# Performance work log

Measured on AMD Instinct MI355X. Metric: run time of the kernel, lower is better.

## Reference

```python
import jax, jax.numpy as jnp
import numpy as np

N_NODES = 100000
N_GRAPHS = 64


def gcn_conv(x, edge_index, edge_weight, W, b):
    # PyG GCNConv: h = W^T x, then out[dst] += norm * h[src], norm = d^-1/2[src]*w*d^-1/2[dst]
    n = x.shape[0]
    loop = jnp.arange(n)
    src = jnp.concatenate([edge_index[0], loop])
    dst = jnp.concatenate([edge_index[1], loop])
    w = jnp.concatenate([edge_weight, jnp.ones((n,), x.dtype)])  # self-loop weight 1
    deg = jax.ops.segment_sum(w, dst, num_segments=n)
    dis = jnp.where(deg > 0, jax.lax.rsqrt(jnp.maximum(deg, 1e-30)), 0.0)
    norm = dis[src] * w * dis[dst]                      # [E+N]
    h = x @ W                                            # [N, d_out]
    msg = h[src] * norm[:, None]                         # gather + scale
    out = jax.ops.segment_sum(msg, dst, num_segments=n)  # scatter-add
    return out + b


def setup_inputs() -> dict:
    key = jax.random.key(0)
    k = jax.random.split(key, 8)
    d_in, d_out = 256, 128
    E = 1600000
    x = jax.random.normal(k[0], (N_NODES, d_in), jnp.float32)
    edge_index = jax.random.randint(k[1], (2, E), 0, N_NODES, jnp.int64)
    edge_weight = jax.random.uniform(k[2], (E,), jnp.float32)
    batch = jnp.sort(jax.random.randint(k[3], (N_NODES,), 0, N_GRAPHS, jnp.int64))
    W_conv = jax.random.normal(k[4], (d_in, d_out), jnp.float32) / np.sqrt(d_in)
    b_conv = jnp.zeros((d_out,), jnp.float32)
    W_lin = jax.random.normal(k[5], (d_out, 1), jnp.float32) / np.sqrt(d_out)
    b_lin = jnp.zeros((1,), jnp.float32)
    return {"x": x, "edge_index": edge_index, "edge_weight": edge_weight,
            "batch": batch, "W_conv": W_conv, "b_conv": b_conv,
            "W_lin": W_lin, "b_lin": b_lin}


def reference(x, edge_index, edge_weight, batch, W_conv, b_conv, W_lin, b_lin):
    h = gcn_conv(x, edge_index, edge_weight, W_conv, b_conv)
    h = jax.nn.relu(h)
    # dropout(p=0.1) treated as identity (eval) for deterministic baseline
    sums = jax.ops.segment_sum(h, batch, num_segments=N_GRAPHS)
    counts = jax.ops.segment_sum(jnp.ones((h.shape[0],), h.dtype), batch,
                                 num_segments=N_GRAPHS)
    pooled = sums / jnp.maximum(counts, 1.0)[:, None]    # [G, d_out]
    logits = pooled @ W_lin + b_lin                       # [G, 1]
    return jax.nn.sigmoid(logits)
```

## Files before the change

kernel.cpp:

```cpp
#include <hip/hip_runtime.h>
#include <hip/hip_bf16.h>
#include <math.h>

#define D_IN 256
#define D_OUT 128
#define WSCALE 1073741824.0f

typedef __bf16 bf16x8 __attribute__((ext_vector_type(8)));
typedef float  f32x4  __attribute__((ext_vector_type(4)));
typedef float  f32x2  __attribute__((ext_vector_type(2)));

__device__ __forceinline__ ushort f2b(float f) {
    unsigned int x = __float_as_uint(f);
    unsigned int r = (x + 0x7FFFu + ((x >> 16) & 1u)) >> 16;
    return (ushort)r;
}
__device__ __forceinline__ f32x2 fp8x2_f32(unsigned u) {
    return __builtin_amdgcn_cvt_pk_f32_fp8(u, false);
}
__device__ __forceinline__ unsigned char f32_fp8(float f) {
    return (unsigned char)(__builtin_amdgcn_cvt_pk_fp8_f32(f, f, 0, false) & 0xFF);
}

__global__ void wt_k(const float* __restrict__ W, ushort* __restrict__ Wtg) {
    int t = blockIdx.x * 256 + threadIdx.x;
    if (t < D_IN * D_OUT) {
        int k = t >> 7, n = t & 127;
        Wtg[n * D_IN + k] = f2b(W[t]);
    }
}

__global__ __launch_bounds__(256, 4) void fused_k(const int* __restrict__ dst,
                                                  const float* __restrict__ w,
                                                  unsigned long long* __restrict__ packed,
                                                  int* __restrict__ pos, int E, int GB,
                                                  const float* __restrict__ X,
                                                  const ushort* __restrict__ Wtg,
                                                  unsigned char* __restrict__ H, int M) {
    const int b = (int)blockIdx.x;
    const bool isg = ((b & 1) == 0) && ((b >> 1) < GB);
    if (!isg) {
        int gb_before = (b + 1) >> 1;
        if (gb_before > GB) gb_before = GB;
        int e0 = (b - gb_before) * 1024 + (int)threadIdx.x;
        #pragma unroll
        for (int i = 0; i < 4; ++i) {
            int e = e0 + i * 256;
            if (e < E) {
                int d = dst[e];
                unsigned long long inc = (1ull << 40) |
                    (unsigned long long)(w[e] * WSCALE);
                unsigned long long old = atomicAdd(&packed[d], inc);
                pos[e] = (int)(old >> 40);
            }
        }
        return;
    }
    extern __shared__ char smem[];
    const int t = threadIdx.x;
    const int brow = (b >> 1) * 64;
    const int wid = t >> 6;
    const int lane = t & 63;
    const int lrow = lane & 15;
    const int lkc = lane >> 4;

    bf16x8 breg[2][8];
    #pragma unroll
    for (int n = 0; n < 2; ++n) {
        int col = wid * 32 + n * 16 + lrow;
        const char* base = (const char*)(Wtg + col * D_IN);
        #pragma unroll
        for (int kk = 0; kk < 8; ++kk)
            breg[n][kk] = *(const bf16x8*)(base + kk * 64 + lkc * 16);
    }

    {
        const float4* x4 = (const float4*)X;
        #pragma unroll
        for (int i = 0; i < 16; ++i) {
            int f = t + 256 * i;
            int row = f >> 6;
            int c4 = f & 63;
            int gr = brow + row;
            if (gr > M - 1) gr = M - 1;
            float4 v = x4[(size_t)gr * 64 + c4];
            ushort4 u;
            u.x = f2b(v.x); u.y = f2b(v.y); u.z = f2b(v.z); u.w = f2b(v.w);
            int phys = row * 512 + (((c4 >> 1) ^ (row & 7)) << 4) + ((c4 & 1) << 3);
            *(ushort4*)(smem + phys) = u;
        }
    }
    __syncthreads();

    f32x4 acc[4][2];
    #pragma unroll
    for (int m = 0; m < 4; ++m)
        #pragma unroll
        for (int n = 0; n < 2; ++n) acc[m][n] = (f32x4){0.f, 0.f, 0.f, 0.f};

    #pragma unroll
    for (int kk = 0; kk < 8; ++kk) {
        bf16x8 a[4];
        #pragma unroll
        for (int m = 0; m < 4; ++m) {
            int row = m * 16 + lrow;
            int chunk = kk * 4 + lkc;
            a[m] = *(const bf16x8*)(smem + row * 512 + ((chunk ^ (row & 7)) << 4));
        }
        #pragma unroll
        for (int m = 0; m < 4; ++m) {
            acc[m][0] = __builtin_amdgcn_mfma_f32_16x16x32_bf16(a[m], breg[0][kk], acc[m][0], 0, 0, 0);
            acc[m][1] = __builtin_amdgcn_mfma_f32_16x16x32_bf16(a[m], breg[1][kk], acc[m][1], 0, 0, 0);
        }
    }

    #pragma unroll
    for (int m = 0; m < 4; ++m) {
        #pragma unroll
        for (int v = 0; v < 4; ++v) {
            int gr = brow + m * 16 + lkc * 4 + v;
            if (gr < M) {
                size_t rb = (size_t)gr * D_OUT;
                H[rb + wid * 32 + lrow]      = f32_fp8(acc[m][0][v]);
                H[rb + wid * 32 + 16 + lrow] = f32_fp8(acc[m][1][v]);
            }
        }
    }
}

__global__ __launch_bounds__(256) void scan1_k(const unsigned long long* __restrict__ packed,
                                               int* __restrict__ row_start,
                                               int* __restrict__ blksum,
                                               float* __restrict__ dis, int N) {
    __shared__ int sdata[256];
    int t = threadIdx.x;
    int base = blockIdx.x * 1024;
    int v[4], s = 0;
    #pragma unroll
    for (int i = 0; i < 4; ++i) {
        int idx = base + t * 4 + i;
        if (idx < N) {
            unsigned long long p = packed[idx];
            int cnt = (int)(p >> 40);
            float deg = 1.0f + (float)(p & ((1ull << 40) - 1)) * (1.0f / WSCALE);
            dis[idx] = rsqrtf(deg);
            v[i] = (cnt + 7) & ~7;
        } else v[i] = 0;
        s += v[i];
    }
    sdata[t] = s;
    __syncthreads();
    #pragma unroll
    for (int off = 1; off < 256; off <<= 1) {
        int x = 0;
        if (t >= off) x = sdata[t - off];
        __syncthreads();
        sdata[t] += x;
        __syncthreads();
    }
    int excl = sdata[t] - s;
    if (t == 255) blksum[blockIdx.x] = sdata[t];
    int run = excl;
    #pragma unroll
    for (int i = 0; i < 4; ++i) {
        int idx = base + t * 4 + i;
        if (idx < N) row_start[idx] = run;
        run += v[i];
    }
}

__global__ __launch_bounds__(256) void scan2_k(const int* __restrict__ blksum,
                                               int* __restrict__ blkpre, int NB,
                                               int* __restrict__ row_start, int N) {
    __shared__ int s[256];
    int t = threadIdx.x;
    int v = (t < NB) ? blksum[t] : 0;
    s[t] = v;
    __syncthreads();
    #pragma unroll
    for (int off = 1; off < 256; off <<= 1) {
        int x = 0;
        if (t >= off) x = s[t - off];
        __syncthreads();
        s[t] += x;
        __syncthreads();
    }
    if (t < NB) blkpre[t] = s[t] - v;
    if (t == NB - 1) row_start[N] = s[t];
}

__global__ void fill_k(const int* __restrict__ src, const int* __restrict__ dst,
                       const float* __restrict__ w, const int* __restrict__ pos,
                       const int* __restrict__ row_start, const int* __restrict__ blkpre,
                       const float* __restrict__ dis,
                       unsigned* __restrict__ csr, int E) {
    int e = blockIdx.x * blockDim.x + threadIdx.x;
    if (e >= E) return;
    int s = src[e];
    int d = dst[e];
    float nm = dis[s] * w[e] * dis[d];
    unsigned rec = ((unsigned)s << 15) | (f2b(nm) & 0x7FFFu);
    csr[row_start[d] + blkpre[d >> 10] + pos[e]] = rec;
}

__global__ __launch_bounds__(256) void agg_pool_k(const int* __restrict__ row_start,
                                                  const int* __restrict__ blkpre,
                                                  const unsigned* __restrict__ csr,
                                                  const unsigned char* __restrict__ h,
                                                  const float* __restrict__ dis,
                                                  const float* __restrict__ bconv,
                                                  const int* __restrict__ batch,
                                                  float* __restrict__ pooled,
                                                  float* __restrict__ counts, int N) {
    int wave = threadIdx.x >> 6;
    int lane = threadIdx.x & 63;
    int c = lane * 2;
    float2 b2 = *(const float2*)&bconv[c];
    int n0 = (blockIdx.x * 4 + wave) * 16;
    if (n0 >= N) return;

    float2 accp = make_float2(0.f, 0.f);
    int curg = -1;
    float gcount = 0.f;

    int nend = n0 + 16;
    if (nend > N) nend = N;

    int rs = row_start[n0] + blkpre[n0 >> 10];

    #pragma unroll 1
    for (int n = n0; n < nend; ++n) {
        int np = n + 1;
        int re = row_start[np] + ((np < N) ? blkpre[np >> 10] : 0);
        float din = dis[n];
        float dn2 = din * din;
        ushort su = *(const ushort*)(h + (size_t)n * D_OUT + c);
        f32x2 sv = fp8x2_f32(su);
        float ax = dn2 * sv[0];
        float ay = dn2 * sv[1];
        #pragma unroll 1
        for (int j = rs; j < re; j += 8) {
            uint4 ra = *(const uint4*)(csr + j);
            uint4 rb = *(const uint4*)(csr + j + 4);
            unsigned rc[8] = {ra.x, ra.y, ra.z, ra.w, rb.x, rb.y, rb.z, rb.w};
            ushort uu[8];
            float nm[8];
            #pragma unroll
            for (int k = 0; k < 8; ++k) {
                nm[k] = __uint_as_float((rc[k] & 0x7FFFu) << 16);
                uu[k] = *(const ushort*)(h + (size_t)((rc[k] >> 15) << 7) + c);
            }
            #pragma unroll
            for (int k = 0; k < 8; ++k) {
                f32x2 hv = fp8x2_f32(uu[k]);
                ax += nm[k] * hv[0];
                ay += nm[k] * hv[1];
            }
        }
        rs = re;
        float vx = fmaxf(ax + b2.x, 0.f);
        float vy = fmaxf(ay + b2.y, 0.f);
        int g = batch[n];
        if (g != curg) {
            if (curg >= 0) {
                atomicAdd(&pooled[curg * D_OUT + c],     accp.x);
                atomicAdd(&pooled[curg * D_OUT + c + 1], accp.y);
                if (lane == 0) atomicAdd(&counts[curg], gcount);
            }
            accp = make_float2(0.f, 0.f);
            gcount = 0.f;
            curg = g;
        }
        accp.x += vx;
        accp.y += vy;
        gcount += 1.f;
    }
    if (curg >= 0) {
        atomicAdd(&pooled[curg * D_OUT + c],     accp.x);
        atomicAdd(&pooled[curg * D_OUT + c + 1], accp.y);
        if (lane == 0) atomicAdd(&counts[curg], gcount);
    }
}

__global__ void head_k(const float* __restrict__ pooled, const float* __restrict__ counts,
                       const float* __restrict__ wlin, const float* __restrict__ blin,
                       float* __restrict__ out, int G) {
    int g = blockIdx.x;
    int lane = threadIdx.x;
    float s = 0.f;
    for (int c = lane; c < D_OUT; c += 64)
        s += pooled[g * D_OUT + c] * wlin[c];
    #pragma unroll
    for (int off = 32; off; off >>= 1) s += __shfl_down(s, off);
    if (lane == 0) {
        float cnt = fmaxf(counts[g], 1.0f);
        float z = s / cnt + blin[0];
        out[g] = 1.0f / (1.0f + expf(-z));
    }
}

extern "C" void kernel_launch(void* const* d_in, const int* in_sizes, int n_in,
                              void* d_out, int out_size, void* d_ws, size_t ws_size,
                              hipStream_t stream) {
    const float* x     = (const float*)d_in[0];
    const int*   ei    = (const int*)  d_in[1];
    const float* ew    = (const float*)d_in[2];
    const int*   batch = (const int*)  d_in[3];
    const float* Wc    = (const float*)d_in[4];
    const float* bc    = (const float*)d_in[5];
    const float* Wl    = (const float*)d_in[6];
    const float* bl    = (const float*)d_in[7];
    float* out = (float*)d_out;

    const int E = in_sizes[2];
    const int N = in_sizes[3];
    const int G = out_size;
    const int NB = (N + 1023) >> 10;
    const int EB = (E + 1023) / 1024;
    const int GB = (N + 63) / 64;
    const int CSR_CAP = E + 8 * N;

    const int* src = ei;
    const int* dst = ei + E;

    unsigned long long* packed = (unsigned long long*)d_ws;
    float*  pooled   = (float*)(packed + N);
    float*  counts   = pooled + (size_t)G * D_OUT;
    unsigned* csr    = (unsigned*)(counts + G);
    int*    pos      = (int*)(csr + CSR_CAP);
    float*  dis      = (float*)(pos + E);
    unsigned char* h = (unsigned char*)(dis + N);
    ushort* Wtg      = (ushort*)(h + (size_t)N * D_OUT);
    int*    row_start= (int*)(Wtg + D_IN * D_OUT);
    int*    blksum   = row_start + N + 1;
    int*    blkpre   = blksum + NB;

    size_t zbytes = (size_t)N * 8 + ((size_t)G * D_OUT + G) * sizeof(float)
                  + (size_t)CSR_CAP * sizeof(unsigned);
    hipMemsetAsync(packed, 0, zbytes, stream);

    wt_k      <<<(D_IN * D_OUT + 255) / 256, 256, 0, stream>>>(Wc, Wtg);

    fused_k   <<<EB + GB, 256, 32768, stream>>>(dst, ew, packed, pos, E, GB,
                                                x, Wtg, h, N);

    scan1_k   <<<NB, 256, 0, stream>>>(packed, row_start, blksum, dis, N);
    scan2_k   <<<1, 256, 0, stream>>>(blksum, blkpre, NB, row_start, N);

    fill_k    <<<(E + 255) / 256, 256, 0, stream>>>(src, dst, ew, pos, row_start, blkpre, dis, csr, E);

    agg_pool_k<<<(N + 63) / 64, 256, 0, stream>>>(row_start, blkpre, csr, h, dis, bc, batch,
                                                  pooled, counts, N);

    head_k    <<<G, 64, 0, stream>>>(pooled, counts, Wl, bl, out, G);
}
```

Before: 210.8 us.

## Replicate degree/count atomics per XCD to keep atomics local to each L2

The degree and count atomic accumulator is replicated once per XCD (eight copies). Each edge block reads its hardware XCC id and does workgroup-scope atomics into its own replica, which avoids cross-die coherence traffic. The scan then merges the eight replicas into per-XCD prefix offsets stored as 16-bit values, and fill_k adds the right offset when placing each CSR entry. This costs an eight-times larger memset and extra reads in the scan. Workgroup scope on global atomics across CUs of the same XCD relies on the shared L2 for correctness, and the 16-bit prefixes assume node degrees stay below 65536.

```diff
diff --git a/kernel.cpp b/kernel.cpp
--- a/kernel.cpp
+++ b/kernel.cpp
@@ -5,6 +5,8 @@
 #define D_IN 256
 #define D_OUT 128
 #define WSCALE 1073741824.0f
+#define NXCD 8
+#define XCC_GETREG_IMM ((31 << 11) | 20)
 
 typedef __bf16 bf16x8 __attribute__((ext_vector_type(8)));
 typedef float  f32x4  __attribute__((ext_vector_type(4)));
@@ -32,7 +34,7 @@
 
 __global__ __launch_bounds__(256, 4) void fused_k(const int* __restrict__ dst,
                                                   const float* __restrict__ w,
-                                                  unsigned long long* __restrict__ packed,
+                                                  unsigned long long* __restrict__ packed8,
                                                   int* __restrict__ pos, int E, int GB,
                                                   const float* __restrict__ X,
                                                   const ushort* __restrict__ Wtg,
@@ -43,6 +45,8 @@
         int gb_before = (b + 1) >> 1;
         if (gb_before > GB) gb_before = GB;
         int e0 = (b - gb_before) * 1024 + (int)threadIdx.x;
+        int xcd = (int)(__builtin_amdgcn_s_getreg(XCC_GETREG_IMM) & 7u);
+        unsigned long long* rep = packed8 + (size_t)xcd * M;
         #pragma unroll
         for (int i = 0; i < 4; ++i) {
             int e = e0 + i * 256;
@@ -50,8 +54,9 @@
                 int d = dst[e];
                 unsigned long long inc = (1ull << 40) |
                     (unsigned long long)(w[e] * WSCALE);
-                unsigned long long old = atomicAdd(&packed[d], inc);
-                pos[e] = (int)(old >> 40);
+                unsigned long long old = __hip_atomic_fetch_add(
+                    &rep[d], inc, __ATOMIC_RELAXED, __HIP_MEMORY_SCOPE_WORKGROUP);
+                pos[e] = (xcd << 27) | (int)(old >> 40);
             }
         }
         return;
@@ -128,10 +133,11 @@
     }
 }
 
-__global__ __launch_bounds__(256) void scan1_k(const unsigned long long* __restrict__ packed,
+__global__ __launch_bounds__(256) void scan1_k(const unsigned long long* __restrict__ packed8,
                                                int* __restrict__ row_start,
                                                int* __restrict__ blksum,
-                                               float* __restrict__ dis, int N) {
+                                               float* __restrict__ dis,
+                                               uint4* __restrict__ xbase, int N) {
     __shared__ int sdata[256];
     int t = threadIdx.x;
     int base = blockIdx.x * 1024;
@@ -140,11 +146,25 @@
     for (int i = 0; i < 4; ++i) {
         int idx = base + t * 4 + i;
         if (idx < N) {
-            unsigned long long p = packed[idx];
-            int cnt = (int)(p >> 40);
-            float deg = 1.0f + (float)(p & ((1ull << 40) - 1)) * (1.0f / WSCALE);
+            unsigned long long ws = 0;
+            unsigned pre[8];
+            unsigned run = 0;
+            #pragma unroll
+            for (int k = 0; k < 8; ++k) {
+                unsigned long long p = packed8[(size_t)k * N + idx];
+                pre[k] = run;
+                run += (unsigned)(p >> 40);
+                ws += p & ((1ull << 40) - 1);
+            }
+            float deg = 1.0f + (float)ws * (1.0f / WSCALE);
             dis[idx] = rsqrtf(deg);
-            v[i] = (cnt + 7) & ~7;
+            uint4 xb;
+            xb.x = pre[0] | (pre[1] << 16);
+            xb.y = pre[2] | (pre[3] << 16);
+            xb.z = pre[4] | (pre[5] << 16);
+            xb.w = pre[6] | (pre[7] << 16);
+            xbase[idx] = xb;
+            v[i] = ((int)run + 7) & ~7;
         } else v[i] = 0;
         s += v[i];
     }
@@ -192,15 +212,20 @@
 __global__ void fill_k(const int* __restrict__ src, const int* __restrict__ dst,
                        const float* __restrict__ w, const int* __restrict__ pos,
                        const int* __restrict__ row_start, const int* __restrict__ blkpre,
+                       const ushort* __restrict__ xbase16,
                        const float* __restrict__ dis,
                        unsigned* __restrict__ csr, int E) {
     int e = blockIdx.x * blockDim.x + threadIdx.x;
     if (e >= E) return;
     int s = src[e];
     int d = dst[e];
+    int p = pos[e];
+    int xcd = ((unsigned)p) >> 27;
+    int local = p & ((1 << 27) - 1);
     float nm = dis[s] * w[e] * dis[d];
     unsigned rec = ((unsigned)s << 15) | (f2b(nm) & 0x7FFFu);
-    csr[row_start[d] + blkpre[d >> 10] + pos[e]] = rec;
+    int slot = row_start[d] + blkpre[d >> 10] + (int)xbase16[(size_t)d * 8 + xcd] + local;
+    csr[slot] = rec;
 }
 
 __global__ __launch_bounds__(256) void agg_pool_k(const int* __restrict__ row_start,
@@ -318,36 +343,38 @@
     const int NB = (N + 1023) >> 10;
     const int EB = (E + 1023) / 1024;
     const int GB = (N + 63) / 64;
-    const int CSR_CAP = E + 8 * N;
+    const int CSR_CAP = E + 8 * N + 16;
 
     const int* src = ei;
     const int* dst = ei + E;
 
-    unsigned long long* packed = (unsigned long long*)d_ws;
-    float*  pooled   = (float*)(packed + N);
+    unsigned long long* packed8 = (unsigned long long*)d_ws;
+    float*  pooled   = (float*)(packed8 + (size_t)NXCD * N);
     float*  counts   = pooled + (size_t)G * D_OUT;
     unsigned* csr    = (unsigned*)(counts + G);
     int*    pos      = (int*)(csr + CSR_CAP);
     float*  dis      = (float*)(pos + E);
     unsigned char* h = (unsigned char*)(dis + N);
     ushort* Wtg      = (ushort*)(h + (size_t)N * D_OUT);
-    int*    row_start= (int*)(Wtg + D_IN * D_OUT);
+    uint4*  xbase    = (uint4*)(Wtg + D_IN * D_OUT);
+    int*    row_start= (int*)(xbase + N);
     int*    blksum   = row_start + N + 1;
     int*    blkpre   = blksum + NB;
 
-    size_t zbytes = (size_t)N * 8 + ((size_t)G * D_OUT + G) * sizeof(float)
+    size_t zbytes = (size_t)NXCD * N * 8 + ((size_t)G * D_OUT + G) * sizeof(float)
                   + (size_t)CSR_CAP * sizeof(unsigned);
-    hipMemsetAsync(packed, 0, zbytes, stream);
+    hipMemsetAsync(packed8, 0, zbytes, stream);
 
     wt_k      <<<(D_IN * D_OUT + 255) / 256, 256, 0, stream>>>(Wc, Wtg);
 
-    fused_k   <<<EB + GB, 256, 32768, stream>>>(dst, ew, packed, pos, E, GB,
+    fused_k   <<<EB + GB, 256, 32768, stream>>>(dst, ew, packed8, pos, E, GB,
                                                 x, Wtg, h, N);
 
-    scan1_k   <<<NB, 256, 0, stream>>>(packed, row_start, blksum, dis, N);
+    scan1_k   <<<NB, 256, 0, stream>>>(packed8, row_start, blksum, dis, xbase, N);
     scan2_k   <<<1, 256, 0, stream>>>(blksum, blkpre, NB, row_start, N);
 
-    fill_k    <<<(E + 255) / 256, 256, 0, stream>>>(src, dst, ew, pos, row_start, blkpre, dis, csr, E);
+    fill_k    <<<(E + 255) / 256, 256, 0, stream>>>(src, dst, ew, pos, row_start, blkpre,
+                                                    (const ushort*)xbase, dis, csr, E);
 
     agg_pool_k<<<(N + 63) / 64, 256, 0, stream>>>(row_start, blkpre, csr, h, dis, bc, batch,
                                                   pooled, counts, N);
```

New measurement: 231.4 us. +9.8%, slower.
